# Optimization experiments

Measured on AMD Instinct MI355X. Metric: run time of the kernel, lower is better.

The kernel has to match this reference:

```python
import jax, jax.numpy as jnp
import numpy as np

D_MODEL = 1024
NUM_HEADS = 16
D_K = D_MODEL // NUM_HEADS
WINDOW = 256


def setup_inputs() -> dict:
    key = jax.random.key(0)
    ks = jax.random.split(key, 11)
    B, S, D = 2, 2048, D_MODEL
    scale = 1.0 / np.sqrt(D)
    inp = {
        "q": jax.random.normal(ks[0], (B, S, D), jnp.float32),
        "k": jax.random.normal(ks[1], (B, S, D), jnp.float32),
        "v": jax.random.normal(ks[2], (B, S, D), jnp.float32),
        "Wq": jax.random.normal(ks[3], (D, D), jnp.float32) * scale,
        "bq": jnp.zeros((D,), jnp.float32),
        "Wk": jax.random.normal(ks[4], (D, D), jnp.float32) * scale,
        "bk": jnp.zeros((D,), jnp.float32),
        "Wv": jax.random.normal(ks[5], (D, D), jnp.float32) * scale,
        "bv": jnp.zeros((D,), jnp.float32),
        "Wo": jax.random.normal(ks[6], (D, D), jnp.float32) * scale,
        "bo": jnp.zeros((D,), jnp.float32),
    }
    return inp


def _split_heads(x):
    B, S, _ = x.shape
    return x.reshape(B, S, NUM_HEADS, D_K).transpose(0, 2, 1, 3)  # [B,H,S,d_k]


def reference(q, k, v, Wq, bq, Wk, bk, Wv, bv, Wo, bo):
    B, S, D = q.shape
    qh = _split_heads(q @ Wq + bq)
    kh = _split_heads(k @ Wk + bk)
    vh = _split_heads(v @ Wv + bv)

    # dense scores then sliding-window band mask (|i-j| <= WINDOW), as in SparseAttention
    scores = jnp.einsum("bhqd,bhkd->bhqk", qh, kh) / jnp.sqrt(jnp.float32(D_K))
    idx = jnp.arange(S)
    band = jnp.abs(idx[:, None] - idx[None, :]) <= WINDOW  # [S,S]
    scores = jnp.where(band[None, None], scores, -jnp.inf)
    attn = jax.nn.softmax(scores, axis=-1)

    out = jnp.einsum("bhqk,bhkd->bhqd", attn, vh)
    out = out.transpose(0, 2, 1, 3).reshape(B, S, D)  # combine heads
    out = out @ Wo + bo
    return out, attn
```

## Files before the change

### kernel.cpp

```cpp
#include <hip/hip_runtime.h>


constexpr int Bb = 2, Ss = 2048, Dd = 1024, Hh = 16, WINw = 256;
constexpr size_t XS_SLAB = (size_t)4096 * 2048;
constexpr size_t WT_SLAB = (size_t)1024 * 2048;
constexpr size_t QB_SLAB = (size_t)4096 * 1024;
constexpr size_t ATTN_BYTES = (size_t)Bb * Hh * Ss * Ss * 4;

typedef short s16x8 __attribute__((ext_vector_type(8)));
typedef float f32x4 __attribute__((ext_vector_type(4)));

typedef __attribute__((address_space(3))) unsigned int lds_uint;
typedef const __attribute__((address_space(1))) unsigned int gbl_uint;

__device__ __forceinline__ void gld_lds16(const void* g, void* l) {
  __builtin_amdgcn_global_load_lds((gbl_uint*)g, (lds_uint*)l, 16, 0, 0);
}

__device__ __forceinline__ void lgkm_barrier() {
  asm volatile("s_waitcnt lgkmcnt(0)" ::: "memory");
  __builtin_amdgcn_s_barrier();
}

__device__ inline unsigned short f2bf(float x) {
  unsigned u = __float_as_uint(x);
  u += 0x7fff + ((u >> 16) & 1);
  return (unsigned short)(u >> 16);
}
__device__ inline float bf2f(unsigned short h) {
  return __uint_as_float(((unsigned)h) << 16);
}

__global__ __launch_bounds__(256) void convert_xw(
    const float* __restrict__ x0, const float* __restrict__ x1,
    const float* __restrict__ x2, unsigned short* __restrict__ Xs,
    const float* __restrict__ w0, const float* __restrict__ w1,
    const float* __restrict__ w2, const float* __restrict__ w3,
    unsigned short* __restrict__ Wt) {
  __shared__ float T[64][65];
  const int id = blockIdx.x;
  const int t = threadIdx.x;
  if (id < 12288) {
    int z = id >> 12;
    int bx = id & 4095;
    const float* src = z == 0 ? x0 : (z == 1 ? x1 : x2);
    unsigned short* dst = Xs + (size_t)z * XS_SLAB;
    size_t idx = ((size_t)bx * 256 + t) * 4;
    int r = (int)(idx >> 10);
    int c = (int)(idx & 1023);
    f32x4 v = *(const f32x4*)&src[idx];
    unsigned short hi[4], lo[4];
#pragma unroll
    for (int i = 0; i < 4; ++i) {
      float vi = v[i];
      hi[i] = f2bf(vi);
      lo[i] = f2bf(vi - bf2f(hi[i]));
    }
    ushort4 h4 = {hi[0], hi[1], hi[2], hi[3]};
    ushort4 l4 = {lo[0], lo[1], lo[2], lo[3]};
    *(ushort4*)&dst[(size_t)r * 2048 + c] = h4;
    *(ushort4*)&dst[(size_t)r * 2048 + 1024 + c] = l4;
  } else {
    int wid = id - 12288;
    int z = wid >> 8;
    int by = (wid >> 4) & 15;
    int bx = wid & 15;
    const float* W = z == 0 ? w0 : (z == 1 ? w1 : (z == 2 ? w2 : w3));
    unsigned short* dst = Wt + (size_t)z * WT_SLAB;
    int k0 = by * 64, n0 = bx * 64;
#pragma unroll
    for (int i = 0; i < 4; ++i) {
      int row = (t >> 4) + i * 16;
      int c4 = (t & 15) * 4;
      f32x4 v = *(const f32x4*)&W[(size_t)(k0 + row) * 1024 + n0 + c4];
      T[row][c4 + 0] = v[0]; T[row][c4 + 1] = v[1];
      T[row][c4 + 2] = v[2]; T[row][c4 + 3] = v[3];
    }
    __syncthreads();
    int n = t >> 2;
    int kc = (t & 3) * 16;
    unsigned short hi[16], lo[16];
#pragma unroll
    for (int j = 0; j < 16; ++j) {
      float x = T[kc + j][n];
      hi[j] = f2bf(x);
      lo[j] = f2bf(x - bf2f(hi[j]));
    }
    size_t base = (size_t)(n0 + n) * 2048 + k0 + kc;
#pragma unroll
    for (int j4 = 0; j4 < 4; ++j4) {
      ushort4 h4 = {hi[j4 * 4], hi[j4 * 4 + 1], hi[j4 * 4 + 2], hi[j4 * 4 + 3]};
      ushort4 l4 = {lo[j4 * 4], lo[j4 * 4 + 1], lo[j4 * 4 + 2], lo[j4 * 4 + 3]};
      *(ushort4*)&dst[base + j4 * 4] = h4;
      *(ushort4*)&dst[base + 1024 + j4 * 4] = l4;
    }
  }
}

__global__ __launch_bounds__(256, 3) void gemm_qkv(
    const unsigned short* __restrict__ Abase,
    const unsigned short* __restrict__ Wtbase,
    unsigned short* __restrict__ Cbase, const float* __restrict__ bb0,
    const float* __restrict__ bb1, const float* __restrict__ bb2,
    float* __restrict__ attnz) {
  __shared__ s16x8 As[2][512];
  __shared__ s16x8 Bs[2][512];
  int z = blockIdx.z;
  const unsigned short* A = Abase + (size_t)z * XS_SLAB;
  const unsigned short* Wt = Wtbase + (size_t)z * WT_SLAB;
  const float* bias = z == 0 ? bb0 : (z == 1 ? bb1 : bb2);
  const float scl = (z == 0) ? 0.125f : 1.0f;

  const int t = threadIdx.x;
  const int lane = t & 63, wave = t >> 6;
  const int wm = wave & 1, wn = wave >> 1;

  const int flat = blockIdx.x + (blockIdx.y << 3);
  const int swz = (flat & 7) * 32 + (flat >> 3);
  const int bm = (swz >> 3) * 128, bn = (swz & 7) * 128;

  const int flat3 = flat + (z << 8);
  const size_t zbase = (size_t)(flat3 * 4 + wave) * 196608;
  char* const az = (char*)attnz;
  const f32x4 zv = {0.f, 0.f, 0.f, 0.f};

  f32x4 acc[4][4] = {};

  const int s0 = t, s1 = t + 256;
  const int r0 = s0 >> 2, c0 = (s0 & 3) ^ ((r0 >> 1) & 3);
  const int r1 = s1 >> 2, c1 = (s1 & 3) ^ ((r1 >> 1) & 3);
  const unsigned short* A0 = A + (size_t)(bm + r0) * 2048 + c0 * 8;
  const unsigned short* A1 = A + (size_t)(bm + r1) * 2048 + c1 * 8;
  const unsigned short* B0 = Wt + (size_t)(bn + r0) * 2048 + c0 * 8;
  const unsigned short* B1 = Wt + (size_t)(bn + r1) * 2048 + c1 * 8;

  const int m15 = lane & 15, q = lane >> 4;

  gld_lds16(A0, &As[0][wave * 64]);
  gld_lds16(A1, &As[0][256 + wave * 64]);
  gld_lds16(B0, &Bs[0][wave * 64]);
  gld_lds16(B1, &Bs[0][256 + wave * 64]);
  __syncthreads();

  int cur = 0;
  for (int kb = 0; kb < 3072; kb += 32) {
    if ((kb & 255) == 0) {
      size_t base = zbase + (size_t)(kb >> 8) * 16384 + (size_t)(lane << 4);
#pragma unroll
      for (int j = 0; j < 16; ++j) {
        size_t off = base + (size_t)j * 1024;
        if (off < ATTN_BYTES)
          __builtin_nontemporal_store(zv, (f32x4*)(az + off));
      }
    }

    const int kn = kb + 32;
    const bool more = (kn < 3072);
    if (more) {
      int asrc = kn < 1024 ? kn : kn - 1024;
      int wsrc = kn < 2048 ? kn : kn - 2048;
      gld_lds16(A0 + asrc, &As[cur ^ 1][wave * 64]);
      gld_lds16(A1 + asrc, &As[cur ^ 1][256 + wave * 64]);
      gld_lds16(B0 + wsrc, &Bs[cur ^ 1][wave * 64]);
      gld_lds16(B1 + wsrc, &Bs[cur ^ 1][256 + wave * 64]);
    }

    s16x8 af[4], bf[4];
#pragma unroll
    for (int mt = 0; mt < 4; ++mt) {
      int r = wm * 64 + mt * 16 + m15;
      af[mt] = As[cur][r * 4 + (q ^ ((r >> 1) & 3))];
    }
#pragma unroll
    for (int nt = 0; nt < 4; ++nt) {
      int r = wn * 64 + nt * 16 + m15;
      bf[nt] = Bs[cur][r * 4 + (q ^ ((r >> 1) & 3))];
    }
#pragma unroll
    for (int mt = 0; mt < 4; ++mt)
#pragma unroll
      for (int nt = 0; nt < 4; ++nt)
        acc[mt][nt] = __builtin_amdgcn_mfma_f32_16x16x32_bf16(
            af[mt], bf[nt], acc[mt][nt], 0, 0, 0);

    if (more) {
      __syncthreads();
      cur ^= 1;
    }
  }

#pragma unroll
  for (int nt = 0; nt < 4; ++nt) {
    int col = bn + wn * 64 + nt * 16 + m15;
    float bv = bias[col];
#pragma unroll
    for (int mt = 0; mt < 4; ++mt) {
      int rowb = bm + wm * 64 + mt * 16 + q * 4;
#pragma unroll
      for (int i = 0; i < 4; ++i) {
        float val = (acc[mt][nt][i] + bv) * scl;
        (Cbase + (size_t)z * QB_SLAB)[(size_t)(rowb + i) * 1024 + col] =
            f2bf(val);
      }
    }
  }
}

__global__ __launch_bounds__(256, 2) void gemm_out(
    const unsigned short* __restrict__ A,
    const unsigned short* __restrict__ Wt,
    float* __restrict__ C, const float* __restrict__ bias) {
  __shared__ s16x8 As[2][256];
  __shared__ s16x8 Bs[2][512];
  const int t = threadIdx.x;
  const int lane = t & 63, wave = t >> 6;
  const int wm = wave & 1, wn = wave >> 1;

  const int flat = blockIdx.x + (blockIdx.y << 3);
  const int swz = (flat & 7) * 64 + (flat >> 3);
  const int bm = (swz >> 3) * 64, bn = (swz & 7) * 128;

  f32x4 acc[2][4] = {};

  const int ra = t >> 2, ca = (t & 3) ^ ((ra >> 1) & 3);
  const int s0 = t, s1 = t + 256;
  const int r0 = s0 >> 2, c0 = (s0 & 3) ^ ((r0 >> 1) & 3);
  const int r1 = s1 >> 2, c1 = (s1 & 3) ^ ((r1 >> 1) & 3);
  const unsigned short* Ap = A + (size_t)(bm + ra) * 2048 + ca * 8;
  const unsigned short* B0 = Wt + (size_t)(bn + r0) * 2048 + c0 * 8;
  const unsigned short* B1 = Wt + (size_t)(bn + r1) * 2048 + c1 * 8;

  const int m15 = lane & 15, q = lane >> 4;

  gld_lds16(Ap, &As[0][wave * 64]);
  gld_lds16(B0, &Bs[0][wave * 64]);
  gld_lds16(B1, &Bs[0][256 + wave * 64]);
  __syncthreads();

  int cur = 0;
  for (int kb = 0; kb < 3072; kb += 32) {
    const int kn = kb + 32;
    if (kn < 3072) {
      int asrc = kn < 1024 ? kn : kn - 1024;
      int wsrc = kn < 2048 ? kn : kn - 2048;
      gld_lds16(Ap + asrc, &As[cur ^ 1][wave * 64]);
      gld_lds16(B0 + wsrc, &Bs[cur ^ 1][wave * 64]);
      gld_lds16(B1 + wsrc, &Bs[cur ^ 1][256 + wave * 64]);
    }

    s16x8 af[2], bf[4];
#pragma unroll
    for (int mt = 0; mt < 2; ++mt) {
      int r = wm * 32 + mt * 16 + m15;
      af[mt] = As[cur][r * 4 + (q ^ ((r >> 1) & 3))];
    }
#pragma unroll
    for (int nt = 0; nt < 4; ++nt) {
      int r = wn * 64 + nt * 16 + m15;
      bf[nt] = Bs[cur][r * 4 + (q ^ ((r >> 1) & 3))];
    }
#pragma unroll
    for (int mt = 0; mt < 2; ++mt)
#pragma unroll
      for (int nt = 0; nt < 4; ++nt)
        acc[mt][nt] = __builtin_amdgcn_mfma_f32_16x16x32_bf16(
            af[mt], bf[nt], acc[mt][nt], 0, 0, 0);

    if (kn < 3072) {
      __syncthreads();
      cur ^= 1;
    }
  }

#pragma unroll
  for (int nt = 0; nt < 4; ++nt) {
    int col = bn + wn * 64 + nt * 16 + m15;
    float bv = bias[col];
#pragma unroll
    for (int mt = 0; mt < 2; ++mt) {
      int rowb = bm + wm * 32 + mt * 16 + q * 4;
#pragma unroll
      for (int i = 0; i < 4; ++i) {
        __builtin_nontemporal_store(
            acc[mt][nt][i] + bv, &C[(size_t)(rowb + i) * 1024 + col]);
      }
    }
  }
}

__global__ __launch_bounds__(256) void transpose_v(
    const unsigned short* __restrict__ Vb, unsigned short* __restrict__ Vt) {
  __shared__ unsigned short T[64][88];
  const int b = blockIdx.z, h = blockIdx.y, s0 = blockIdx.x * 64;
  const int t = threadIdx.x;
  {
    int row = t >> 2, part = t & 3;
    const unsigned short* src =
        Vb + (size_t)(b * Ss + s0 + row) * 1024 + h * 64 + part * 16;
    s16x8 v0 = *(const s16x8*)src;
    s16x8 v1 = *(const s16x8*)(src + 8);
    *(s16x8*)&T[row][part * 16] = v0;
    *(s16x8*)&T[row][part * 16 + 8] = v1;
  }
  __syncthreads();
  {
    int d = t & 63, sw = t >> 6;
    unsigned short tmp[16];
#pragma unroll
    for (int i = 0; i < 16; ++i) tmp[i] = T[sw * 16 + i][d];
    unsigned short* dst =
        Vt + ((size_t)((b * Hh + h) * 64 + d)) * 2048 + s0 + sw * 16;
    *(s16x8*)dst = *(const s16x8*)&tmp[0];
    *(s16x8*)(dst + 8) = *(const s16x8*)&tmp[8];
  }
}

constexpr int SW3 = 556;
__global__ __launch_bounds__(256) void attn_v6(
    const unsigned short* __restrict__ Qb, const unsigned short* __restrict__ Kb,
    const unsigned short* __restrict__ Vt, float* __restrict__ attn,
    unsigned short* __restrict__ XsAO) {
  __shared__ float P[16 * SW3];
  const int t = threadIdx.x;
  const int lane = t & 63, wave = t >> 6;
  const int m15 = lane & 15, quad = lane >> 4;
  const int bid0 = blockIdx.x;
  const int bid = (bid0 & 7) * 512 + (bid0 >> 3);
  const int qt = bid & 127, h = (bid >> 7) & 15, b = bid >> 11;
  const int q0 = qt * 16;
  int jlo = q0 - WINw; if (jlo < 0) jlo = 0;
  int jhi = q0 + 15 + WINw; if (jhi > Ss - 1) jhi = Ss - 1;
  const int ncols = jhi - jlo + 1;
  const int ntiles = ncols >> 4;

  {
    const unsigned short* qrow =
        Qb + (size_t)(b * Ss + q0 + m15) * 1024 + h * 64 + quad * 8;
    s16x8 aq0 = *(const s16x8*)qrow;
    s16x8 aq1 = *(const s16x8*)(qrow + 32);
    for (int nt = wave; nt < ntiles; nt += 4) {
      const unsigned short* krow =
          Kb + (size_t)(b * Ss + jlo + nt * 16 + m15) * 1024 + h * 64 + quad * 8;
      s16x8 b0 = *(const s16x8*)krow;
      s16x8 b1 = *(const s16x8*)(krow + 32);
      f32x4 c = {0.f, 0.f, 0.f, 0.f};
      __builtin_amdgcn_s_setprio(1);
      c = __builtin_amdgcn_mfma_f32_16x16x32_bf16(aq0, b0, c, 0, 0, 0);
      c = __builtin_amdgcn_mfma_f32_16x16x32_bf16(aq1, b1, c, 0, 0, 0);
      __builtin_amdgcn_s_setprio(0);
      float* pp = &P[(quad * 4) * SW3 + nt * 16 + m15];
#pragma unroll
      for (int i = 0; i < 4; ++i) pp[i * SW3] = c[i];
    }
  }
  lgkm_barrier();

  {
#pragma unroll
    for (int ri = 0; ri < 4; ++ri) {
      const int r = wave * 4 + ri;
      const int qq = q0 + r;
      int lo = qq - WINw; if (lo < 0) lo = 0;
      int hi = qq + WINw; if (hi > Ss - 1) hi = Ss - 1;
      const int clo = lo - jlo, chi = hi - jlo;
      float sv[9];
      bool ib[9];
      float m = -1e30f;
#pragma unroll
      for (int k2 = 0; k2 < 9; ++k2) {
        int c = k2 * 64 + lane;
        bool inb = (c >= clo) && (c <= chi);
        ib[k2] = inb;
        float vv = inb ? P[r * SW3 + c] : -1e30f;
        sv[k2] = vv;
        m = fmaxf(m, vv);
      }
#pragma unroll
      for (int off = 32; off; off >>= 1) m = fmaxf(m, __shfl_xor(m, off, 64));
      float e[9], l = 0.f;
#pragma unroll
      for (int k2 = 0; k2 < 9; ++k2) { e[k2] = __expf(sv[k2] - m); l += e[k2]; }
#pragma unroll
      for (int off = 32; off; off >>= 1) l += __shfl_xor(l, off, 64);
      const float inv = 1.f / l;
      unsigned short* pb = (unsigned short*)&P[r * SW3];
      float* arow = attn + ((size_t)((b * Hh + h) * Ss + qq)) * Ss + jlo;
#pragma unroll
      for (int k2 = 0; k2 < 9; ++k2) {
        int c = k2 * 64 + lane;
        float w = ib[k2] ? e[k2] * inv : 0.f;
        if (c < 544) pb[c] = f2bf(w);
        if (c < ncols) __builtin_nontemporal_store(w, &arow[c]);
      }
    }
  }
  lgkm_barrier();

  {
    const int ntk = (ncols + 31) >> 5;
    const unsigned short* vtrow =
        Vt + ((size_t)((b * Hh + h) * 64 + wave * 16 + m15)) * 2048 + jlo +
        quad * 8;
    f32x4 o = {0.f, 0.f, 0.f, 0.f};
    const unsigned short* pbrow = (const unsigned short*)&P[m15 * SW3];
    for (int ks = 0; ks < ntk; ++ks) {
      s16x8 af = *(const s16x8*)&pbrow[ks * 32 + quad * 8];
      s16x8 bf = *(const s16x8*)(vtrow + ks * 32);
      __builtin_amdgcn_s_setprio(1);
      o = __builtin_amdgcn_mfma_f32_16x16x32_bf16(af, bf, o, 0, 0, 0);
      __builtin_amdgcn_s_setprio(0);
    }
    const int dcol = h * 64 + wave * 16 + m15;
#pragma unroll
    for (int i = 0; i < 4; ++i) {
      int row = q0 + quad * 4 + i;
      unsigned short hi = f2bf(o[i]);
      unsigned short lo = f2bf(o[i] - bf2f(hi));
      unsigned short* dst = XsAO + (size_t)(b * Ss + row) * 2048 + dcol;
      dst[0] = hi;
      dst[1024] = lo;
    }
  }
}

extern "C" void kernel_launch(void* const* d_in, const int* in_sizes, int n_in,
                              void* d_out, int out_size, void* d_ws,
                              size_t ws_size, hipStream_t stream) {
  const float* q  = (const float*)d_in[0];
  const float* k  = (const float*)d_in[1];
  const float* v  = (const float*)d_in[2];
  const float* Wq = (const float*)d_in[3];
  const float* bq = (const float*)d_in[4];
  const float* Wk = (const float*)d_in[5];
  const float* bk = (const float*)d_in[6];
  const float* Wv = (const float*)d_in[7];
  const float* bv = (const float*)d_in[8];
  const float* Wo = (const float*)d_in[9];
  const float* bo = (const float*)d_in[10];

  float* out = (float*)d_out;
  float* attn = out + (size_t)Bb * Ss * Dd;

  unsigned short* Xs   = (unsigned short*)d_ws;
  unsigned short* XsAO = Xs + 3 * XS_SLAB;
  unsigned short* Wt   = XsAO + XS_SLAB;
  unsigned short* Qb   = Wt + 4 * WT_SLAB;
  unsigned short* Kb   = Qb + QB_SLAB;
  unsigned short* Vb   = Kb + QB_SLAB;
  unsigned short* Vt   = Vb + QB_SLAB;

  hipLaunchKernelGGL(convert_xw, dim3(12288 + 1024), dim3(256), 0, stream,
                     q, k, v, Xs, Wq, Wk, Wv, Wo, Wt);
  hipLaunchKernelGGL(gemm_qkv, dim3(8, 32, 3), dim3(256), 0, stream,
                     Xs, Wt, Qb, bq, bk, bv, attn);
  hipLaunchKernelGGL(transpose_v, dim3(32, 16, 2), dim3(256), 0, stream,
                     Vb, Vt);
  hipLaunchKernelGGL(attn_v6, dim3(Bb * Hh * (Ss / 16)), dim3(256), 0, stream,
                     Qb, Kb, Vt, attn, XsAO);
  hipLaunchKernelGGL(gemm_out, dim3(8, 64, 1), dim3(256), 0, stream,
                     XsAO, Wt + 3 * WT_SLAB, out, bo);
}
```

Before: 782.2 us.

## Drop low-part correction for Q/K projections and move attn zero-fill into attention

```diff
diff --git a/kernel.cpp b/kernel.cpp
--- a/kernel.cpp
+++ b/kernel.cpp
@@ -5,7 +5,6 @@
 constexpr size_t XS_SLAB = (size_t)4096 * 2048;
 constexpr size_t WT_SLAB = (size_t)1024 * 2048;
 constexpr size_t QB_SLAB = (size_t)4096 * 1024;
-constexpr size_t ATTN_BYTES = (size_t)Bb * Hh * Ss * Ss * 4;
 
 typedef short s16x8 __attribute__((ext_vector_type(8)));
 typedef float f32x4 __attribute__((ext_vector_type(4)));
@@ -59,7 +58,8 @@
     ushort4 h4 = {hi[0], hi[1], hi[2], hi[3]};
     ushort4 l4 = {lo[0], lo[1], lo[2], lo[3]};
     *(ushort4*)&dst[(size_t)r * 2048 + c] = h4;
-    *(ushort4*)&dst[(size_t)r * 2048 + 1024 + c] = l4;
+    if (z == 2)
+      *(ushort4*)&dst[(size_t)r * 2048 + 1024 + c] = l4;
   } else {
     int wid = id - 12288;
     int z = wid >> 8;
@@ -101,8 +101,7 @@
     const unsigned short* __restrict__ Abase,
     const unsigned short* __restrict__ Wtbase,
     unsigned short* __restrict__ Cbase, const float* __restrict__ bb0,
-    const float* __restrict__ bb1, const float* __restrict__ bb2,
-    float* __restrict__ attnz) {
+    const float* __restrict__ bb1, const float* __restrict__ bb2) {
   __shared__ s16x8 As[2][512];
   __shared__ s16x8 Bs[2][512];
   int z = blockIdx.z;
@@ -110,6 +109,7 @@
   const unsigned short* Wt = Wtbase + (size_t)z * WT_SLAB;
   const float* bias = z == 0 ? bb0 : (z == 1 ? bb1 : bb2);
   const float scl = (z == 0) ? 0.125f : 1.0f;
+  const int KMAX = (z == 2) ? 3072 : 2048;
 
   const int t = threadIdx.x;
   const int lane = t & 63, wave = t >> 6;
@@ -118,11 +118,6 @@
   const int flat = blockIdx.x + (blockIdx.y << 3);
   const int swz = (flat & 7) * 32 + (flat >> 3);
   const int bm = (swz >> 3) * 128, bn = (swz & 7) * 128;
-
-  const int flat3 = flat + (z << 8);
-  const size_t zbase = (size_t)(flat3 * 4 + wave) * 196608;
-  char* const az = (char*)attnz;
-  const f32x4 zv = {0.f, 0.f, 0.f, 0.f};
 
   f32x4 acc[4][4] = {};
 
@@ -143,19 +138,9 @@
   __syncthreads();
 
   int cur = 0;
-  for (int kb = 0; kb < 3072; kb += 32) {
-    if ((kb & 255) == 0) {
-      size_t base = zbase + (size_t)(kb >> 8) * 16384 + (size_t)(lane << 4);
-#pragma unroll
-      for (int j = 0; j < 16; ++j) {
-        size_t off = base + (size_t)j * 1024;
-        if (off < ATTN_BYTES)
-          __builtin_nontemporal_store(zv, (f32x4*)(az + off));
-      }
-    }
-
+  for (int kb = 0; kb < KMAX; kb += 32) {
     const int kn = kb + 32;
-    const bool more = (kn < 3072);
+    const bool more = (kn < KMAX);
     if (more) {
       int asrc = kn < 1024 ? kn : kn - 1024;
       int wsrc = kn < 2048 ? kn : kn - 2048;
@@ -316,7 +301,7 @@
 }
 
 constexpr int SW3 = 556;
-__global__ __launch_bounds__(256) void attn_v6(
+__global__ __launch_bounds__(256) void attn_v7(
     const unsigned short* __restrict__ Qb, const unsigned short* __restrict__ Kb,
     const unsigned short* __restrict__ Vt, float* __restrict__ attn,
     unsigned short* __restrict__ XsAO) {
@@ -356,6 +341,7 @@
   lgkm_barrier();
 
   {
+    const f32x4 zv = {0.f, 0.f, 0.f, 0.f};
 #pragma unroll
     for (int ri = 0; ri < 4; ++ri) {
       const int r = wave * 4 + ri;
@@ -384,13 +370,20 @@
       for (int off = 32; off; off >>= 1) l += __shfl_xor(l, off, 64);
       const float inv = 1.f / l;
       unsigned short* pb = (unsigned short*)&P[r * SW3];
-      float* arow = attn + ((size_t)((b * Hh + h) * Ss + qq)) * Ss + jlo;
+      float* arow0 = attn + ((size_t)((b * Hh + h) * Ss + qq)) * Ss;
+      float* arow = arow0 + jlo;
 #pragma unroll
       for (int k2 = 0; k2 < 9; ++k2) {
         int c = k2 * 64 + lane;
         float w = ib[k2] ? e[k2] * inv : 0.f;
         if (c < 544) pb[c] = f2bf(w);
         if (c < ncols) __builtin_nontemporal_store(w, &arow[c]);
+      }
+#pragma unroll
+      for (int i = 0; i < 8; ++i) {
+        int col = i * 256 + lane * 4;
+        if (col < jlo || col >= jlo + ncols)
+          __builtin_nontemporal_store(zv, (f32x4*)&arow0[col]);
       }
     }
   }
@@ -452,10 +445,10 @@
   hipLaunchKernelGGL(convert_xw, dim3(12288 + 1024), dim3(256), 0, stream,
                      q, k, v, Xs, Wq, Wk, Wv, Wo, Wt);
   hipLaunchKernelGGL(gemm_qkv, dim3(8, 32, 3), dim3(256), 0, stream,
-                     Xs, Wt, Qb, bq, bk, bv, attn);
+                     Xs, Wt, Qb, bq, bk, bv);
   hipLaunchKernelGGL(transpose_v, dim3(32, 16, 2), dim3(256), 0, stream,
                      Vb, Vt);
-  hipLaunchKernelGGL(attn_v6, dim3(Bb * Hh * (Ss / 16)), dim3(256), 0, stream,
+  hipLaunchKernelGGL(attn_v7, dim3(Bb * Hh * (Ss / 16)), dim3(256), 0, stream,
                      Qb, Kb, Vt, attn, XsAO);
   hipLaunchKernelGGL(gemm_out, dim3(8, 64, 1), dim3(256), 0, stream,
                      XsAO, Wt + 3 * WT_SLAB, out, bo);
```

Result: faster. 759.7 us (-2.9%).
